# Performance work log

Hardware: AMD Instinct MI355X
Metric: run time of the kernel (lower is better)

The kernel has to match this reference:

```python
import jax, jax.numpy as jnp
import numpy as np

DIM, HEADS, K = 128, 4, 7
HD = DIM // HEADS


def _nbr_idx(n, k):
    # NATTEN boundary-clamped neighborhood (dilation=1): window start clamped to [0, n-k]
    i = np.arange(n)
    start = np.clip(i - k // 2, 0, n - k)
    idx = start[:, None] + np.arange(k)[None, :]          # (n, k) absolute neighbor index
    rel = idx - i[:, None] + (k - 1)                      # (n, k) index into 2k-1 rpb axis
    return jnp.asarray(idx), jnp.asarray(rel)


def _ln(x, w, b, eps=1e-5):
    mu = jnp.mean(x, -1, keepdims=True)
    var = jnp.var(x, -1, keepdims=True)
    return (x - mu) * jax.lax.rsqrt(var + eps) * w + b


def setup_inputs() -> dict:
    key = jax.random.key(0)
    ks = jax.random.split(key, 16)
    B, H, W, C = 1, 128, 128, DIM
    f = jax.random.normal
    inp = {
        'x': f(ks[0], (B, H, W, C), jnp.float32),
        'y': f(ks[1], (B, H, W, C), jnp.float32),
        'qv_w': f(ks[2], (2 * C, C), jnp.float32) * 0.02,
        'qv_b': jnp.zeros((2 * C,), jnp.float32),
        'k_w': f(ks[3], (C, C), jnp.float32) * 0.02,
        'k_b': jnp.zeros((C,), jnp.float32),
        'rpb': f(ks[4], (HEADS, 2 * K - 1, 2 * K - 1), jnp.float32) * 0.02,
        'proj_w': f(ks[5], (C, C), jnp.float32) * 0.02,
        'proj_b': jnp.zeros((C,), jnp.float32),
        'n1_w': jnp.ones((C,), jnp.float32),
        'n1_b': jnp.zeros((C,), jnp.float32),
        'n2_w': jnp.ones((C,), jnp.float32),
        'n2_b': jnp.zeros((C,), jnp.float32),
        'fc1_w': f(ks[6], (4 * C, C), jnp.float32) * 0.02,
        'fc1_b': jnp.zeros((4 * C,), jnp.float32),
        'fc2_w': f(ks[7], (C, 4 * C), jnp.float32) * 0.02,
        'fc2_b': jnp.zeros((C,), jnp.float32),
    }
    return inp


def _block(x, y, qv_w, qv_b, k_w, k_b, rpb, proj_w, proj_b,
           n1_w, n1_b, n2_w, n2_b, fc1_w, fc1_b, fc2_w, fc2_b):
    B, H, W, C = x.shape
    scale = HD ** -0.5
    # ---- CrossNat2D attention on norm1(x) vs y ----
    xn = _ln(x, n1_w, n1_b)
    qv = xn @ qv_w.T + qv_b                               # (B,H,W,2C)
    q = qv[..., :C].reshape(B, H, W, HEADS, HD) * scale
    v = qv[..., C:].reshape(B, H, W, HEADS, HD)
    k = (y @ k_w.T + k_b).reshape(B, H, W, HEADS, HD)

    idx_h, rel_h = _nbr_idx(H, K)
    idx_w, rel_w = _nbr_idx(W, K)
    # gather neighborhoods: (B, H, K, W, K, HEADS, HD)
    k_nbr = k[:, idx_h][:, :, :, idx_w]
    v_nbr = v[:, idx_h][:, :, :, idx_w]

    # attention logits over KxK neighborhood
    attn = jnp.einsum('bijhd,biajchd->bijhac', q, k_nbr)  # (B,H,W,heads,K,K)
    bias = rpb[:, rel_h][..., rel_w]                      # (heads,H,K,W,K)
    attn = attn + jnp.transpose(bias, (1, 3, 0, 2, 4))    # broadcast over B
    attn = jax.nn.softmax(attn.reshape(B, H, W, HEADS, K * K), axis=-1)
    attn = attn.reshape(B, H, W, HEADS, K, K)

    out = jnp.einsum('bijhac,biajchd->bijhd', attn, v_nbr).reshape(B, H, W, C)
    out = out @ proj_w.T + proj_b

    x = x + out
    # ---- MLP ----
    h = _ln(x, n2_w, n2_b) @ fc1_w.T + fc1_b
    h = jax.nn.gelu(h, approximate=False) @ fc2_w.T + fc2_b
    return x + h


def reference(x, y, qv_w, qv_b, k_w, k_b, rpb, proj_w, proj_b,
              n1_w, n1_b, n2_w, n2_b, fc1_w, fc1_b, fc2_w, fc2_b):
    return _block(x, y, qv_w, qv_b, k_w, k_b, rpb, proj_w, proj_b,
                  n1_w, n1_b, n2_w, n2_b, fc1_w, fc1_b, fc2_w, fc2_b)
```

## Files before the change

kernel.cpp:

```cpp
#include <hip/hip_runtime.h>
#include <hip/hip_bf16.h>


#define N_PIX 16384
#define C 128
#define HEADS 4
#define HD 32
#define HW 128

typedef __hip_bfloat16 bf16;
typedef __attribute__((ext_vector_type(8))) short bf16x8;
typedef __attribute__((ext_vector_type(4))) float f32x4;

__device__ __forceinline__ short f2bs(float f) {
    bf16 h = __float2bfloat16(f);
    return (short)__bfloat16_as_ushort(h);
}
__device__ __forceinline__ float bs2f(short s) {
    __hip_bfloat16_raw r; r.x = (unsigned short)s;
    return __bfloat162float(__hip_bfloat16(r));
}
__device__ __forceinline__ float gelu_f(float v) {
    const float z = 1.5957691216f * (v + 0.044715f * v * v * v);
    return v / (1.f + __expf(-z));
}
__device__ __forceinline__ unsigned int pack2(float a, float b) {
    return (unsigned int)(unsigned short)f2bs(a) |
           ((unsigned int)(unsigned short)f2bs(b) << 16);
}

__global__ __launch_bounds__(256) void k_wconv(
    const float* __restrict__ qv_w, const float* __restrict__ k_w,
    const float* __restrict__ proj_w, const float* __restrict__ fc1_w,
    const float* __restrict__ fc2_w,
    short* __restrict__ wqv, short* __restrict__ wk, short* __restrict__ wproj,
    short* __restrict__ wfc1, short* __restrict__ wfc2) {
    const int i = blockIdx.x * 256 + threadIdx.x;
    if (i < 32768) wqv[i] = f2bs(qv_w[i]);
    if (i < 16384) { wk[i] = f2bs(k_w[i]); wproj[i] = f2bs(proj_w[i]); }
    if (i < 65536) { wfc1[i] = f2bs(fc1_w[i]); wfc2[i] = f2bs(fc2_w[i]); }
}

__global__ __launch_bounds__(512, 6) void k_qkv(
    const float* __restrict__ x, const float* __restrict__ y,
    const short* __restrict__ wqv, const float* __restrict__ qv_b,
    const short* __restrict__ wk, const float* __restrict__ k_b,
    const float* __restrict__ n1_w, const float* __restrict__ n1_b,
    bf16* __restrict__ qb, bf16* __restrict__ vb, bf16* __restrict__ kb,
    bf16* __restrict__ xbo) {
    __shared__ float xr[32][132];
    __shared__ short xn[32][136];
    __shared__ short yb[32][136];
    __shared__ float muA[32], riA[32];
    const int t = threadIdx.x;
    const int pix0 = (blockIdx.x & 7) * 2048 + (blockIdx.x >> 3) * 32;
    for (int e = t; e < 1024; e += 512) {
        const int r = e >> 5, c4 = (e & 31) * 4;
        const float4 xv = *(const float4*)(x + (size_t)(pix0 + r) * C + c4);
        *(float4*)&xr[r][c4] = xv;
        uint2 xp; xp.x = pack2(xv.x, xv.y); xp.y = pack2(xv.z, xv.w);
        *(uint2*)(xbo + (size_t)(pix0 + r) * C + c4) = xp;
        const float4 yv = *(const float4*)(y + (size_t)(pix0 + r) * C + c4);
        uint2 yp; yp.x = pack2(yv.x, yv.y); yp.y = pack2(yv.z, yv.w);
        *(uint2*)&yb[r][c4] = yp;
    }
    __syncthreads();
    if (t < 256) {
        const int r = t >> 3, s = t & 7;
        float sm = 0.f, sq = 0.f;
        for (int i = 0; i < 16; i++) { float v = xr[r][s * 16 + i]; sm += v; sq += v * v; }
        for (int m = 1; m < 8; m <<= 1) { sm += __shfl_xor(sm, m, 64); sq += __shfl_xor(sq, m, 64); }
        if (s == 0) {
            const float mu = sm * (1.f / 128.f);
            const float var = sq * (1.f / 128.f) - mu * mu;
            muA[r] = mu; riA[r] = rsqrtf(var + 1e-5f);
        }
    }
    __syncthreads();
    for (int e = t; e < 32 * 128; e += 512) {
        const int r = e >> 7, c = e & 127;
        xn[r][c] = f2bs((xr[r][c] - muA[r]) * riA[r] * n1_w[c] + n1_b[c]);
    }
    __syncthreads();
    const int wave = t >> 6, lane = t & 63, quad = lane >> 4, l15 = lane & 15;
    const int mt = wave & 1, wv = wave >> 1;
    const float scale = 0.1767766952966369f;
    {
        bf16x8 aA[4];
#pragma unroll
        for (int kt = 0; kt < 4; kt++)
            aA[kt] = *(const bf16x8*)&xn[mt * 16 + l15][kt * 32 + quad * 8];
#pragma unroll
        for (int s = 0; s < 4; s++) {
            const int n = (wv * 4 + s) * 16 + l15;
            f32x4 acc = {0.f, 0.f, 0.f, 0.f};
#pragma unroll
            for (int kt = 0; kt < 4; kt++) {
                bf16x8 b = *(const bf16x8*)&wqv[n * C + kt * 32 + quad * 8];
                acc = __builtin_amdgcn_mfma_f32_16x16x32_bf16(aA[kt], b, acc, 0, 0, 0);
            }
            const float bias = qv_b[n];
#pragma unroll
            for (int r = 0; r < 4; r++) {
                const int m = mt * 16 + quad * 4 + r;
                const float v = acc[r] + bias;
                if (n < C) qb[(pix0 + m) * C + n] = __float2bfloat16(v * scale);
                else       vb[(pix0 + m) * C + (n - C)] = __float2bfloat16(v);
            }
        }
    }
    {
        bf16x8 aY[4];
#pragma unroll
        for (int kt = 0; kt < 4; kt++)
            aY[kt] = *(const bf16x8*)&yb[mt * 16 + l15][kt * 32 + quad * 8];
        const int n0 = (wv * 2) * 16 + l15, n1 = (wv * 2 + 1) * 16 + l15;
        f32x4 a0 = {0.f, 0.f, 0.f, 0.f}, a1 = {0.f, 0.f, 0.f, 0.f};
#pragma unroll
        for (int kt = 0; kt < 4; kt++) {
            bf16x8 b0 = *(const bf16x8*)&wk[n0 * C + kt * 32 + quad * 8];
            bf16x8 b1 = *(const bf16x8*)&wk[n1 * C + kt * 32 + quad * 8];
            a0 = __builtin_amdgcn_mfma_f32_16x16x32_bf16(aY[kt], b0, a0, 0, 0, 0);
            a1 = __builtin_amdgcn_mfma_f32_16x16x32_bf16(aY[kt], b1, a1, 0, 0, 0);
        }
        const float b0s = k_b[n0], b1s = k_b[n1];
#pragma unroll
        for (int r = 0; r < 4; r++) {
            const int m = mt * 16 + quad * 4 + r;
            kb[(pix0 + m) * C + n0] = __float2bfloat16(a0[r] + b0s);
            kb[(pix0 + m) * C + n1] = __float2bfloat16(a1[r] + b1s);
        }
    }
}

__global__ __launch_bounds__(512, 2) void k_fam(
    const bf16* __restrict__ qb, const bf16* __restrict__ kb,
    const bf16* __restrict__ vb, const float* __restrict__ rpb,
    const bf16* __restrict__ xb,
    const short* __restrict__ wproj, const float* __restrict__ proj_b,
    const float* __restrict__ n2_w, const float* __restrict__ n2_b,
    const short* __restrict__ wfc1, const float* __restrict__ fc1_b,
    const short* __restrict__ wfc2, const float* __restrict__ fc2_b,
    float* __restrict__ out) {
    __shared__ short KP[19008];
    __shared__ short Vl[19008];
    __shared__ float muA[32], riA[32];
    short* const Pm  = KP;
    short* const aoL = KP;
    short* const x1b = KP + 4352;
    short* const xnb = KP + 8704;
    short* const hb  = Vl;
    const int t = threadIdx.x;
    const int wave = t >> 6, lane = t & 63, quad = lane >> 4, l15 = lane & 15;
    const int h = wave & 3, mt = wave >> 2;
    const int s_ = blockIdx.x >> 3;
    const int i0 = ((blockIdx.x & 7) * 2 + (s_ >> 5)) * 8;
    const int j0 = (s_ & 31) * 4;
    const int rs = min(max(i0 - 3, 0), 114);
    const int cs = min(max(j0 - 3, 0), 118);
    const int mA = mt * 16 + l15;
    const int pA = (i0 + (mA >> 2)) * HW + j0 + (mA & 3);
    const bf16x8 aQ = *(const bf16x8*)(qb + (size_t)pA * C + h * HD + quad * 8);
    const int nR0 = h * 16 + l15, nR1 = (h + 4) * 16 + l15;
    short xres0[4], xres1[4];
#pragma unroll
    for (int r = 0; r < 4; r++) {
        const int m = mt * 16 + quad * 4 + r;
        const int p = (i0 + (m >> 2)) * HW + j0 + (m & 3);
        xres0[r] = *(const short*)(xb + (size_t)p * C + nR0);
        xres1[r] = *(const short*)(xb + (size_t)p * C + nR1);
    }
    for (int u = t; u < 140 * 16 * 2; u += 512) {
        const int tv = (u >= 2240) ? 1 : 0;
        const int uu = tv ? u - 2240 : u;
        const int r = uu >> 4, seg = uu & 15;
        const size_t g = (size_t)((rs + r / 10) * HW + cs + r % 10) * C + seg * 8;
        const uint4 d = *(const uint4*)((tv ? vb : kb) + g);
        *(uint4*)&(tv ? Vl : KP)[r * 132 + seg * 8] = d;
    }
    __syncthreads();
    f32x4 S[9];
#pragma unroll
    for (int nt = 0; nt < 9; nt++) {
        const bf16x8 bK = *(const bf16x8*)&KP[(nt * 16 + l15) * 132 + h * HD + quad * 8];
        f32x4 z = {0.f, 0.f, 0.f, 0.f};
        S[nt] = __builtin_amdgcn_mfma_f32_16x16x32_bf16(aQ, bK, z, 0, 0, 0);
    }
    const float* rpbh = rpb + h * 169;
    float smx[4];
#pragma unroll
    for (int r = 0; r < 4; r++) {
        const int m = mt * 16 + quad * 4 + r;
        const int i = i0 + (m >> 2), j = j0 + (m & 3);
        const int shi = min(max(i - 3, 0), 121);
        const int swj = min(max(j - 3, 0), 121);
        float best = -1e30f;
#pragma unroll
        for (int nt = 0; nt < 9; nt++) {
            const int nb = nt * 16 + l15;
            const int ai = rs + nb / 10, aj = cs + nb % 10;
            const bool valid = (nb < 140) & (ai >= shi) & (ai <= shi + 6) & (aj >= swj) & (aj <= swj + 6);
            const int ri = min(max(ai - i + 6, 0), 12);
            const int rj = min(max(aj - j + 6, 0), 12);
            const float v = valid ? (S[nt][r] + rpbh[ri * 13 + rj]) : -1e30f;
            S[nt][r] = v;
            best = fmaxf(best, v);
        }
        for (int msk = 1; msk < 16; msk <<= 1) best = fmaxf(best, __shfl_xor(best, msk, 64));
        float s = 0.f;
#pragma unroll
        for (int nt = 0; nt < 9; nt++) {
            const float e = __expf(S[nt][r] - best);
            S[nt][r] = e;
            s += e;
        }
        for (int msk = 1; msk < 16; msk <<= 1) s += __shfl_xor(s, msk, 64);
        smx[r] = 1.f / s;
    }
    __syncthreads();
#pragma unroll
    for (int r = 0; r < 4; r++) {
        short* prow = &Pm[(wave * 16 + quad * 4 + r) * 144];
#pragma unroll
        for (int nt = 0; nt < 9; nt++)
            prow[nt * 16 + l15] = f2bs(S[nt][r] * smx[r]);
    }
    f32x4 O0 = {0.f, 0.f, 0.f, 0.f}, O1 = {0.f, 0.f, 0.f, 0.f};
#pragma unroll
    for (int kt = 0; kt < 4; kt++) {
        const bf16x8 aP = *(const bf16x8*)&Pm[(wave * 16 + l15) * 144 + kt * 32 + quad * 8];
#pragma unroll
        for (int nt2 = 0; nt2 < 2; nt2++) {
            const int ch = h * HD + nt2 * 16 + l15;
            const int base = (kt * 32 + quad * 8) * 132 + ch;
            bf16x8 bV;
#pragma unroll
            for (int jj = 0; jj < 8; jj++) bV[jj] = Vl[base + jj * 132];
            if (nt2 == 0) O0 = __builtin_amdgcn_mfma_f32_16x16x32_bf16(aP, bV, O0, 0, 0, 0);
            else          O1 = __builtin_amdgcn_mfma_f32_16x16x32_bf16(aP, bV, O1, 0, 0, 0);
        }
    }
    {
        const bf16x8 aP = *(const bf16x8*)&Pm[(wave * 16 + l15) * 144 + 128 + quad * 8];
#pragma unroll
        for (int nt2 = 0; nt2 < 2; nt2++) {
            const int ch = h * HD + nt2 * 16 + l15;
            bf16x8 bV = {0, 0, 0, 0, 0, 0, 0, 0};
            if (quad == 0) {
                const int base = 128 * 132 + ch;
#pragma unroll
                for (int jj = 0; jj < 8; jj++) bV[jj] = Vl[base + jj * 132];
            } else if (quad == 1) {
                const int base = 136 * 132 + ch;
#pragma unroll
                for (int jj = 0; jj < 4; jj++) bV[jj] = Vl[base + jj * 132];
            }
            if (nt2 == 0) O0 = __builtin_amdgcn_mfma_f32_16x16x32_bf16(aP, bV, O0, 0, 0, 0);
            else          O1 = __builtin_amdgcn_mfma_f32_16x16x32_bf16(aP, bV, O1, 0, 0, 0);
        }
    }
    __syncthreads();
#pragma unroll
    for (int r = 0; r < 4; r++) {
        const int m = mt * 16 + quad * 4 + r;
        aoL[m * 136 + h * HD + l15] = f2bs(O0[r]);
        aoL[m * 136 + h * HD + 16 + l15] = f2bs(O1[r]);
    }
    __syncthreads();
    {
        bf16x8 aO[4];
#pragma unroll
        for (int kt = 0; kt < 4; kt++)
            aO[kt] = *(const bf16x8*)&aoL[(mt * 16 + l15) * 136 + kt * 32 + quad * 8];
        f32x4 a0 = {0.f, 0.f, 0.f, 0.f}, a1 = {0.f, 0.f, 0.f, 0.f};
#pragma unroll
        for (int kt = 0; kt < 4; kt++) {
            bf16x8 b0 = *(const bf16x8*)&wproj[nR0 * C + kt * 32 + quad * 8];
            bf16x8 b1 = *(const bf16x8*)&wproj[nR1 * C + kt * 32 + quad * 8];
            a0 = __builtin_amdgcn_mfma_f32_16x16x32_bf16(aO[kt], b0, a0, 0, 0, 0);
            a1 = __builtin_amdgcn_mfma_f32_16x16x32_bf16(aO[kt], b1, a1, 0, 0, 0);
        }
        const float b0s = proj_b[nR0], b1s = proj_b[nR1];
#pragma unroll
        for (int r = 0; r < 4; r++) {
            const int m = mt * 16 + quad * 4 + r;
            x1b[m * 136 + nR0] = f2bs(bs2f(xres0[r]) + a0[r] + b0s);
            x1b[m * 136 + nR1] = f2bs(bs2f(xres1[r]) + a1[r] + b1s);
        }
    }
    __syncthreads();
    if (t < 256) {
        const int r = t >> 3, s = t & 7;
        float sm = 0.f, sq = 0.f;
        for (int i = 0; i < 16; i++) { float v = bs2f(x1b[r * 136 + s * 16 + i]); sm += v; sq += v * v; }
        for (int m = 1; m < 8; m <<= 1) { sm += __shfl_xor(sm, m, 64); sq += __shfl_xor(sq, m, 64); }
        if (s == 0) {
            const float mu = sm * (1.f / 128.f);
            const float var = sq * (1.f / 128.f) - mu * mu;
            muA[r] = mu; riA[r] = rsqrtf(var + 1e-5f);
        }
    }
    __syncthreads();
    for (int e = t; e < 32 * 128; e += 512) {
        const int r = e >> 7, c = e & 127;
        xnb[r * 136 + c] = f2bs((bs2f(x1b[r * 136 + c]) - muA[r]) * riA[r] * n2_w[c] + n2_b[c]);
    }
    __syncthreads();
    {
        bf16x8 aX[4];
#pragma unroll
        for (int kt = 0; kt < 4; kt++)
            aX[kt] = *(const bf16x8*)&xnb[(mt * 16 + l15) * 136 + kt * 32 + quad * 8];
#pragma unroll
        for (int a = 0; a < 4; a++) {
            const int n0 = (h + 8 * a) * 16 + l15, n1 = (h + 8 * a + 4) * 16 + l15;
            f32x4 a0 = {0.f, 0.f, 0.f, 0.f}, a1 = {0.f, 0.f, 0.f, 0.f};
#pragma unroll
            for (int kt = 0; kt < 4; kt++) {
                bf16x8 b0 = *(const bf16x8*)&wfc1[n0 * C + kt * 32 + quad * 8];
                bf16x8 b1 = *(const bf16x8*)&wfc1[n1 * C + kt * 32 + quad * 8];
                a0 = __builtin_amdgcn_mfma_f32_16x16x32_bf16(aX[kt], b0, a0, 0, 0, 0);
                a1 = __builtin_amdgcn_mfma_f32_16x16x32_bf16(aX[kt], b1, a1, 0, 0, 0);
            }
            const float b0s = fc1_b[n0], b1s = fc1_b[n1];
#pragma unroll
            for (int r = 0; r < 4; r++) {
                const int m = mt * 16 + quad * 4 + r;
                hb[m * 520 + n0] = f2bs(gelu_f(a0[r] + b0s));
                hb[m * 520 + n1] = f2bs(gelu_f(a1[r] + b1s));
            }
        }
    }
    __syncthreads();
    {
        f32x4 a0 = {0.f, 0.f, 0.f, 0.f}, a1 = {0.f, 0.f, 0.f, 0.f};
#pragma unroll
        for (int kt = 0; kt < 16; kt++) {
            const bf16x8 aP = *(const bf16x8*)&hb[(mt * 16 + l15) * 520 + kt * 32 + quad * 8];
            bf16x8 b0 = *(const bf16x8*)&wfc2[nR0 * 512 + kt * 32 + quad * 8];
            bf16x8 b1 = *(const bf16x8*)&wfc2[nR1 * 512 + kt * 32 + quad * 8];
            a0 = __builtin_amdgcn_mfma_f32_16x16x32_bf16(aP, b0, a0, 0, 0, 0);
            a1 = __builtin_amdgcn_mfma_f32_16x16x32_bf16(aP, b1, a1, 0, 0, 0);
        }
        const float b0s = fc2_b[nR0], b1s = fc2_b[nR1];
#pragma unroll
        for (int r = 0; r < 4; r++) {
            const int m = mt * 16 + quad * 4 + r;
            const int p = (i0 + (m >> 2)) * HW + j0 + (m & 3);
            out[(size_t)p * C + nR0] = a0[r] + b0s + bs2f(x1b[m * 136 + nR0]);
            out[(size_t)p * C + nR1] = a1[r] + b1s + bs2f(x1b[m * 136 + nR1]);
        }
    }
}

extern "C" void kernel_launch(void* const* d_in, const int* in_sizes, int n_in,
                              void* d_out, int out_size, void* d_ws, size_t ws_size,
                              hipStream_t stream) {
    const float* x      = (const float*)d_in[0];
    const float* y      = (const float*)d_in[1];
    const float* qv_w   = (const float*)d_in[2];
    const float* qv_b   = (const float*)d_in[3];
    const float* k_w    = (const float*)d_in[4];
    const float* k_b    = (const float*)d_in[5];
    const float* rpb    = (const float*)d_in[6];
    const float* proj_w = (const float*)d_in[7];
    const float* proj_b = (const float*)d_in[8];
    const float* n1_w   = (const float*)d_in[9];
    const float* n1_b   = (const float*)d_in[10];
    const float* n2_w   = (const float*)d_in[11];
    const float* n2_b   = (const float*)d_in[12];
    const float* fc1_w  = (const float*)d_in[13];
    const float* fc1_b  = (const float*)d_in[14];
    const float* fc2_w  = (const float*)d_in[15];
    const float* fc2_b  = (const float*)d_in[16];
    float* out = (float*)d_out;

    bf16* qb  = (bf16*)d_ws;
    bf16* vb  = qb + (size_t)N_PIX * C;
    bf16* kb  = vb + (size_t)N_PIX * C;
    bf16* xb  = kb + (size_t)N_PIX * C;
    short* wqv  = (short*)(xb + (size_t)N_PIX * C);
    short* wk   = wqv + 32768;
    short* wproj= wk + 16384;
    short* wfc1 = wproj + 16384;
    short* wfc2 = wfc1 + 65536;

    k_wconv<<<256, 256, 0, stream>>>(qv_w, k_w, proj_w, fc1_w, fc2_w,
                                     wqv, wk, wproj, wfc1, wfc2);
    k_qkv<<<512, 512, 0, stream>>>(x, y, wqv, qv_b, wk, k_b, n1_w, n1_b,
                                   qb, vb, kb, xb);
    k_fam<<<512, 512, 0, stream>>>(qb, kb, vb, rpb, xb, wproj, proj_b, n2_w, n2_b,
                                   wfc1, fc1_b, wfc2, fc2_b, out);
}
```

Before: 162.7 us.

## Split fused attention+MLP kernel into separate attention and MLP kernels with smaller tiles

The fused attention/projection/MLP kernel becomes two kernels. k_attn handles 4x4 pixel tiles with 256 threads and reuses one shared buffer for K and then V, staging V through registers. k_mlp reads the fp32 residual from the output buffer and applies LN2, fc1, GELU, fc2 and the residual. k_qkv now uses 16-pixel blocks and no longer writes a bf16 copy of x; the residual is read in fp32 instead. The aim is smaller LDS footprint, higher occupancy and a tighter attention halo (100 neighbours instead of 140), at the cost of an extra fp32 round trip of the intermediate through global memory and one more launch.

```diff
diff --git a/kernel.cpp b/kernel.cpp
--- a/kernel.cpp
+++ b/kernel.cpp
@@ -41,31 +41,28 @@
     if (i < 65536) { wfc1[i] = f2bs(fc1_w[i]); wfc2[i] = f2bs(fc2_w[i]); }
 }
 
-__global__ __launch_bounds__(512, 6) void k_qkv(
+__global__ __launch_bounds__(256, 4) void k_qkv(
     const float* __restrict__ x, const float* __restrict__ y,
     const short* __restrict__ wqv, const float* __restrict__ qv_b,
     const short* __restrict__ wk, const float* __restrict__ k_b,
     const float* __restrict__ n1_w, const float* __restrict__ n1_b,
-    bf16* __restrict__ qb, bf16* __restrict__ vb, bf16* __restrict__ kb,
-    bf16* __restrict__ xbo) {
-    __shared__ float xr[32][132];
-    __shared__ short xn[32][136];
-    __shared__ short yb[32][136];
-    __shared__ float muA[32], riA[32];
+    bf16* __restrict__ qb, bf16* __restrict__ vb, bf16* __restrict__ kb) {
+    __shared__ float xr[16][132];
+    __shared__ short xn[16][136];
+    __shared__ short yl[16][136];
+    __shared__ float muA[16], riA[16];
     const int t = threadIdx.x;
-    const int pix0 = (blockIdx.x & 7) * 2048 + (blockIdx.x >> 3) * 32;
-    for (int e = t; e < 1024; e += 512) {
+    const int pix0 = (blockIdx.x & 7) * 2048 + (blockIdx.x >> 3) * 16;
+    for (int e = t; e < 512; e += 256) {
         const int r = e >> 5, c4 = (e & 31) * 4;
         const float4 xv = *(const float4*)(x + (size_t)(pix0 + r) * C + c4);
         *(float4*)&xr[r][c4] = xv;
-        uint2 xp; xp.x = pack2(xv.x, xv.y); xp.y = pack2(xv.z, xv.w);
-        *(uint2*)(xbo + (size_t)(pix0 + r) * C + c4) = xp;
         const float4 yv = *(const float4*)(y + (size_t)(pix0 + r) * C + c4);
         uint2 yp; yp.x = pack2(yv.x, yv.y); yp.y = pack2(yv.z, yv.w);
-        *(uint2*)&yb[r][c4] = yp;
-    }
-    __syncthreads();
-    if (t < 256) {
+        *(uint2*)&yl[r][c4] = yp;
+    }
+    __syncthreads();
+    if (t < 128) {
         const int r = t >> 3, s = t & 7;
         float sm = 0.f, sq = 0.f;
         for (int i = 0; i < 16; i++) { float v = xr[r][s * 16 + i]; sm += v; sq += v * v; }
@@ -77,22 +74,21 @@
         }
     }
     __syncthreads();
-    for (int e = t; e < 32 * 128; e += 512) {
+    for (int e = t; e < 2048; e += 256) {
         const int r = e >> 7, c = e & 127;
         xn[r][c] = f2bs((xr[r][c] - muA[r]) * riA[r] * n1_w[c] + n1_b[c]);
     }
     __syncthreads();
     const int wave = t >> 6, lane = t & 63, quad = lane >> 4, l15 = lane & 15;
-    const int mt = wave & 1, wv = wave >> 1;
     const float scale = 0.1767766952966369f;
     {
         bf16x8 aA[4];
 #pragma unroll
         for (int kt = 0; kt < 4; kt++)
-            aA[kt] = *(const bf16x8*)&xn[mt * 16 + l15][kt * 32 + quad * 8];
+            aA[kt] = *(const bf16x8*)&xn[l15][kt * 32 + quad * 8];
 #pragma unroll
         for (int s = 0; s < 4; s++) {
-            const int n = (wv * 4 + s) * 16 + l15;
+            const int n = (wave * 4 + s) * 16 + l15;
             f32x4 acc = {0.f, 0.f, 0.f, 0.f};
 #pragma unroll
             for (int kt = 0; kt < 4; kt++) {
@@ -102,10 +98,10 @@
             const float bias = qv_b[n];
 #pragma unroll
             for (int r = 0; r < 4; r++) {
-                const int m = mt * 16 + quad * 4 + r;
+                const int m = quad * 4 + r;
                 const float v = acc[r] + bias;
-                if (n < C) qb[(pix0 + m) * C + n] = __float2bfloat16(v * scale);
-                else       vb[(pix0 + m) * C + (n - C)] = __float2bfloat16(v);
+                if (n < C) qb[(size_t)(pix0 + m) * C + n] = __float2bfloat16(v * scale);
+                else       vb[(size_t)(pix0 + m) * C + (n - C)] = __float2bfloat16(v);
             }
         }
     }
@@ -113,8 +109,8 @@
         bf16x8 aY[4];
 #pragma unroll
         for (int kt = 0; kt < 4; kt++)
-            aY[kt] = *(const bf16x8*)&yb[mt * 16 + l15][kt * 32 + quad * 8];
-        const int n0 = (wv * 2) * 16 + l15, n1 = (wv * 2 + 1) * 16 + l15;
+            aY[kt] = *(const bf16x8*)&yl[l15][kt * 32 + quad * 8];
+        const int n0 = (wave * 2) * 16 + l15, n1 = (wave * 2 + 1) * 16 + l15;
         f32x4 a0 = {0.f, 0.f, 0.f, 0.f}, a1 = {0.f, 0.f, 0.f, 0.f};
 #pragma unroll
         for (int kt = 0; kt < 4; kt++) {
@@ -126,80 +122,86 @@
         const float b0s = k_b[n0], b1s = k_b[n1];
 #pragma unroll
         for (int r = 0; r < 4; r++) {
-            const int m = mt * 16 + quad * 4 + r;
-            kb[(pix0 + m) * C + n0] = __float2bfloat16(a0[r] + b0s);
-            kb[(pix0 + m) * C + n1] = __float2bfloat16(a1[r] + b1s);
-        }
-    }
-}
-
-__global__ __launch_bounds__(512, 2) void k_fam(
+            const int m = quad * 4 + r;
+            kb[(size_t)(pix0 + m) * C + n0] = __float2bfloat16(a0[r] + b0s);
+            kb[(size_t)(pix0 + m) * C + n1] = __float2bfloat16(a1[r] + b1s);
+        }
+    }
+}
+
+__global__ __launch_bounds__(256, 3) void k_attn(
     const bf16* __restrict__ qb, const bf16* __restrict__ kb,
     const bf16* __restrict__ vb, const float* __restrict__ rpb,
-    const bf16* __restrict__ xb,
+    const float* __restrict__ x,
     const short* __restrict__ wproj, const float* __restrict__ proj_b,
-    const float* __restrict__ n2_w, const float* __restrict__ n2_b,
-    const short* __restrict__ wfc1, const float* __restrict__ fc1_b,
-    const short* __restrict__ wfc2, const float* __restrict__ fc2_b,
     float* __restrict__ out) {
-    __shared__ short KP[19008];
-    __shared__ short Vl[19008];
-    __shared__ float muA[32], riA[32];
-    short* const Pm  = KP;
-    short* const aoL = KP;
-    short* const x1b = KP + 4352;
-    short* const xnb = KP + 8704;
-    short* const hb  = Vl;
+    __shared__ short U[112 * 132];
+    __shared__ short Pb[64 * 120];
+    __shared__ short aoL[16 * 136];
     const int t = threadIdx.x;
     const int wave = t >> 6, lane = t & 63, quad = lane >> 4, l15 = lane & 15;
-    const int h = wave & 3, mt = wave >> 2;
-    const int s_ = blockIdx.x >> 3;
-    const int i0 = ((blockIdx.x & 7) * 2 + (s_ >> 5)) * 8;
-    const int j0 = (s_ & 31) * 4;
-    const int rs = min(max(i0 - 3, 0), 114);
+    const int h = wave;
+    const int tile = (blockIdx.x & 7) * 128 + (blockIdx.x >> 3);
+    const int i0 = (tile >> 5) * 4, j0 = (tile & 31) * 4;
+    const int rs = min(max(i0 - 3, 0), 118);
     const int cs = min(max(j0 - 3, 0), 118);
-    const int mA = mt * 16 + l15;
-    const int pA = (i0 + (mA >> 2)) * HW + j0 + (mA & 3);
+    const int pA = (i0 + (l15 >> 2)) * HW + j0 + (l15 & 3);
     const bf16x8 aQ = *(const bf16x8*)(qb + (size_t)pA * C + h * HD + quad * 8);
     const int nR0 = h * 16 + l15, nR1 = (h + 4) * 16 + l15;
-    short xres0[4], xres1[4];
+    float xres0[4], xres1[4];
 #pragma unroll
     for (int r = 0; r < 4; r++) {
-        const int m = mt * 16 + quad * 4 + r;
+        const int m = quad * 4 + r;
         const int p = (i0 + (m >> 2)) * HW + j0 + (m & 3);
-        xres0[r] = *(const short*)(xb + (size_t)p * C + nR0);
-        xres1[r] = *(const short*)(xb + (size_t)p * C + nR1);
-    }
-    for (int u = t; u < 140 * 16 * 2; u += 512) {
-        const int tv = (u >= 2240) ? 1 : 0;
-        const int uu = tv ? u - 2240 : u;
-        const int r = uu >> 4, seg = uu & 15;
-        const size_t g = (size_t)((rs + r / 10) * HW + cs + r % 10) * C + seg * 8;
-        const uint4 d = *(const uint4*)((tv ? vb : kb) + g);
-        *(uint4*)&(tv ? Vl : KP)[r * 132 + seg * 8] = d;
-    }
-    __syncthreads();
-    f32x4 S[9];
-#pragma unroll
-    for (int nt = 0; nt < 9; nt++) {
-        const bf16x8 bK = *(const bf16x8*)&KP[(nt * 16 + l15) * 132 + h * HD + quad * 8];
+        xres0[r] = x[(size_t)p * C + nR0];
+        xres1[r] = x[(size_t)p * C + nR1];
+    }
+    uint4 vst[7];
+#pragma unroll
+    for (int it = 0; it < 7; ++it) {
+        const int u = t + it * 256;
+        const int r = u >> 4, seg = u & 15;
+        const int sr = min(r, 99);
+        const size_t g = (size_t)((rs + sr / 10) * HW + cs + sr % 10) * C + seg * 8;
+        *(uint4*)&U[r * 132 + seg * 8] = *(const uint4*)(kb + g);
+        vst[it] = *(const uint4*)(vb + g);
+    }
+    __syncthreads();
+    f32x4 S[7];
+#pragma unroll
+    for (int nt = 0; nt < 7; nt++) {
+        const bf16x8 bK = *(const bf16x8*)&U[(nt * 16 + l15) * 132 + h * HD + quad * 8];
         f32x4 z = {0.f, 0.f, 0.f, 0.f};
         S[nt] = __builtin_amdgcn_mfma_f32_16x16x32_bf16(aQ, bK, z, 0, 0, 0);
     }
+    __syncthreads();
+#pragma unroll
+    for (int it = 0; it < 7; ++it) {
+        const int u = t + it * 256;
+        const int r = u >> 4, seg = u & 15;
+        *(uint4*)&U[r * 132 + seg * 8] = vst[it];
+    }
     const float* rpbh = rpb + h * 169;
+    int aiA[7], ajA[7];
+#pragma unroll
+    for (int nt = 0; nt < 7; nt++) {
+        const int nb = nt * 16 + l15;
+        aiA[nt] = rs + nb / 10;
+        ajA[nt] = cs + nb % 10;
+    }
     float smx[4];
 #pragma unroll
     for (int r = 0; r < 4; r++) {
-        const int m = mt * 16 + quad * 4 + r;
+        const int m = quad * 4 + r;
         const int i = i0 + (m >> 2), j = j0 + (m & 3);
         const int shi = min(max(i - 3, 0), 121);
         const int swj = min(max(j - 3, 0), 121);
         float best = -1e30f;
 #pragma unroll
-        for (int nt = 0; nt < 9; nt++) {
+        for (int nt = 0; nt < 7; nt++) {
             const int nb = nt * 16 + l15;
-            const int ai = rs + nb / 10, aj = cs + nb % 10;
-            const bool valid = (nb < 140) & (ai >= shi) & (ai <= shi + 6) & (aj >= swj) & (aj <= swj + 6);
+            const int ai = aiA[nt], aj = ajA[nt];
+            const bool valid = (nb < 100) & (ai >= shi) & (ai <= shi + 6) & (aj >= swj) & (aj <= swj + 6);
             const int ri = min(max(ai - i + 6, 0), 12);
             const int rj = min(max(aj - j + 6, 0), 12);
             const float v = valid ? (S[nt][r] + rpbh[ri * 13 + rj]) : -1e30f;
@@ -209,7 +211,7 @@
         for (int msk = 1; msk < 16; msk <<= 1) best = fmaxf(best, __shfl_xor(best, msk, 64));
         float s = 0.f;
 #pragma unroll
-        for (int nt = 0; nt < 9; nt++) {
+        for (int nt = 0; nt < 7; nt++) {
             const float e = __expf(S[nt][r] - best);
             S[nt][r] = e;
             s += e;
@@ -217,82 +219,93 @@
         for (int msk = 1; msk < 16; msk <<= 1) s += __shfl_xor(s, msk, 64);
         smx[r] = 1.f / s;
     }
-    __syncthreads();
 #pragma unroll
     for (int r = 0; r < 4; r++) {
-        short* prow = &Pm[(wave * 16 + quad * 4 + r) * 144];
-#pragma unroll
-        for (int nt = 0; nt < 9; nt++)
-            prow[nt * 16 + l15] = f2bs(S[nt][r] * smx[r]);
-    }
+        short* prow = &Pb[(h * 16 + quad * 4 + r) * 120];
+#pragma unroll
+        for (int nt = 0; nt < 7; nt++) prow[nt * 16 + l15] = f2bs(S[nt][r] * smx[r]);
+    }
+    __syncthreads();
     f32x4 O0 = {0.f, 0.f, 0.f, 0.f}, O1 = {0.f, 0.f, 0.f, 0.f};
 #pragma unroll
-    for (int kt = 0; kt < 4; kt++) {
-        const bf16x8 aP = *(const bf16x8*)&Pm[(wave * 16 + l15) * 144 + kt * 32 + quad * 8];
+    for (int kt = 0; kt < 3; kt++) {
+        const bf16x8 aP = *(const bf16x8*)&Pb[(h * 16 + l15) * 120 + kt * 32 + quad * 8];
 #pragma unroll
         for (int nt2 = 0; nt2 < 2; nt2++) {
             const int ch = h * HD + nt2 * 16 + l15;
             const int base = (kt * 32 + quad * 8) * 132 + ch;
             bf16x8 bV;
 #pragma unroll
-            for (int jj = 0; jj < 8; jj++) bV[jj] = Vl[base + jj * 132];
+            for (int jj = 0; jj < 8; jj++) bV[jj] = U[base + jj * 132];
             if (nt2 == 0) O0 = __builtin_amdgcn_mfma_f32_16x16x32_bf16(aP, bV, O0, 0, 0, 0);
             else          O1 = __builtin_amdgcn_mfma_f32_16x16x32_bf16(aP, bV, O1, 0, 0, 0);
         }
     }
     {
-        const bf16x8 aP = *(const bf16x8*)&Pm[(wave * 16 + l15) * 144 + 128 + quad * 8];
+        bf16x8 aP = {0, 0, 0, 0, 0, 0, 0, 0};
+        if (quad < 2) aP = *(const bf16x8*)&Pb[(h * 16 + l15) * 120 + 96 + quad * 8];
 #pragma unroll
         for (int nt2 = 0; nt2 < 2; nt2++) {
             const int ch = h * HD + nt2 * 16 + l15;
             bf16x8 bV = {0, 0, 0, 0, 0, 0, 0, 0};
-            if (quad == 0) {
-                const int base = 128 * 132 + ch;
-#pragma unroll
-                for (int jj = 0; jj < 8; jj++) bV[jj] = Vl[base + jj * 132];
-            } else if (quad == 1) {
-                const int base = 136 * 132 + ch;
-#pragma unroll
-                for (int jj = 0; jj < 4; jj++) bV[jj] = Vl[base + jj * 132];
+            if (quad < 2) {
+                const int base = (96 + quad * 8) * 132 + ch;
+#pragma unroll
+                for (int jj = 0; jj < 8; jj++) bV[jj] = U[base + jj * 132];
             }
             if (nt2 == 0) O0 = __builtin_amdgcn_mfma_f32_16x16x32_bf16(aP, bV, O0, 0, 0, 0);
             else          O1 = __builtin_amdgcn_mfma_f32_16x16x32_bf16(aP, bV, O1, 0, 0, 0);
         }
     }
-    __syncthreads();
 #pragma unroll
     for (int r = 0; r < 4; r++) {
-        const int m = mt * 16 + quad * 4 + r;
+        const int m = quad * 4 + r;
         aoL[m * 136 + h * HD + l15] = f2bs(O0[r]);
         aoL[m * 136 + h * HD + 16 + l15] = f2bs(O1[r]);
     }
     __syncthreads();
-    {
-        bf16x8 aO[4];
-#pragma unroll
-        for (int kt = 0; kt < 4; kt++)
-            aO[kt] = *(const bf16x8*)&aoL[(mt * 16 + l15) * 136 + kt * 32 + quad * 8];
-        f32x4 a0 = {0.f, 0.f, 0.f, 0.f}, a1 = {0.f, 0.f, 0.f, 0.f};
-#pragma unroll
-        for (int kt = 0; kt < 4; kt++) {
-            bf16x8 b0 = *(const bf16x8*)&wproj[nR0 * C + kt * 32 + quad * 8];
-            bf16x8 b1 = *(const bf16x8*)&wproj[nR1 * C + kt * 32 + quad * 8];
-            a0 = __builtin_amdgcn_mfma_f32_16x16x32_bf16(aO[kt], b0, a0, 0, 0, 0);
-            a1 = __builtin_amdgcn_mfma_f32_16x16x32_bf16(aO[kt], b1, a1, 0, 0, 0);
-        }
-        const float b0s = proj_b[nR0], b1s = proj_b[nR1];
-#pragma unroll
-        for (int r = 0; r < 4; r++) {
-            const int m = mt * 16 + quad * 4 + r;
-            x1b[m * 136 + nR0] = f2bs(bs2f(xres0[r]) + a0[r] + b0s);
-            x1b[m * 136 + nR1] = f2bs(bs2f(xres1[r]) + a1[r] + b1s);
-        }
-    }
-    __syncthreads();
-    if (t < 256) {
+    bf16x8 aO[4];
+#pragma unroll
+    for (int kt = 0; kt < 4; kt++)
+        aO[kt] = *(const bf16x8*)&aoL[l15 * 136 + kt * 32 + quad * 8];
+    f32x4 a0 = {0.f, 0.f, 0.f, 0.f}, a1 = {0.f, 0.f, 0.f, 0.f};
+#pragma unroll
+    for (int kt = 0; kt < 4; kt++) {
+        bf16x8 b0 = *(const bf16x8*)&wproj[nR0 * C + kt * 32 + quad * 8];
+        bf16x8 b1 = *(const bf16x8*)&wproj[nR1 * C + kt * 32 + quad * 8];
+        a0 = __builtin_amdgcn_mfma_f32_16x16x32_bf16(aO[kt], b0, a0, 0, 0, 0);
+        a1 = __builtin_amdgcn_mfma_f32_16x16x32_bf16(aO[kt], b1, a1, 0, 0, 0);
+    }
+    const float b0s = proj_b[nR0], b1s = proj_b[nR1];
+#pragma unroll
+    for (int r = 0; r < 4; r++) {
+        const int m = quad * 4 + r;
+        const int p = (i0 + (m >> 2)) * HW + j0 + (m & 3);
+        out[(size_t)p * C + nR0] = xres0[r] + a0[r] + b0s;
+        out[(size_t)p * C + nR1] = xres1[r] + a1[r] + b1s;
+    }
+}
+
+__global__ __launch_bounds__(256, 4) void k_mlp(
+    const float* __restrict__ n2_w, const float* __restrict__ n2_b,
+    const short* __restrict__ wfc1, const float* __restrict__ fc1_b,
+    const short* __restrict__ wfc2, const float* __restrict__ fc2_b,
+    float* __restrict__ out) {
+    __shared__ float x1l[16][132];
+    __shared__ short xnb[16][136];
+    __shared__ short hb[16 * 520];
+    __shared__ float muA[16], riA[16];
+    const int t = threadIdx.x;
+    const int pix0 = (blockIdx.x & 7) * 2048 + (blockIdx.x >> 3) * 16;
+    for (int e = t; e < 512; e += 256) {
+        const int r = e >> 5, c4 = (e & 31) * 4;
+        *(float4*)&x1l[r][c4] = *(const float4*)(out + (size_t)(pix0 + r) * C + c4);
+    }
+    __syncthreads();
+    if (t < 128) {
         const int r = t >> 3, s = t & 7;
         float sm = 0.f, sq = 0.f;
-        for (int i = 0; i < 16; i++) { float v = bs2f(x1b[r * 136 + s * 16 + i]); sm += v; sq += v * v; }
+        for (int i = 0; i < 16; i++) { float v = x1l[r][s * 16 + i]; sm += v; sq += v * v; }
         for (int m = 1; m < 8; m <<= 1) { sm += __shfl_xor(sm, m, 64); sq += __shfl_xor(sq, m, 64); }
         if (s == 0) {
             const float mu = sm * (1.f / 128.f);
@@ -301,54 +314,52 @@
         }
     }
     __syncthreads();
-    for (int e = t; e < 32 * 128; e += 512) {
+    for (int e = t; e < 2048; e += 256) {
         const int r = e >> 7, c = e & 127;
-        xnb[r * 136 + c] = f2bs((bs2f(x1b[r * 136 + c]) - muA[r]) * riA[r] * n2_w[c] + n2_b[c]);
-    }
-    __syncthreads();
+        xnb[r][c] = f2bs((x1l[r][c] - muA[r]) * riA[r] * n2_w[c] + n2_b[c]);
+    }
+    __syncthreads();
+    const int wave = t >> 6, lane = t & 63, quad = lane >> 4, l15 = lane & 15;
     {
         bf16x8 aX[4];
 #pragma unroll
         for (int kt = 0; kt < 4; kt++)
-            aX[kt] = *(const bf16x8*)&xnb[(mt * 16 + l15) * 136 + kt * 32 + quad * 8];
-#pragma unroll
-        for (int a = 0; a < 4; a++) {
-            const int n0 = (h + 8 * a) * 16 + l15, n1 = (h + 8 * a + 4) * 16 + l15;
-            f32x4 a0 = {0.f, 0.f, 0.f, 0.f}, a1 = {0.f, 0.f, 0.f, 0.f};
+            aX[kt] = *(const bf16x8*)&xnb[l15][kt * 32 + quad * 8];
+#pragma unroll
+        for (int a = 0; a < 8; a++) {
+            const int n = (wave * 8 + a) * 16 + l15;
+            f32x4 acc = {0.f, 0.f, 0.f, 0.f};
 #pragma unroll
             for (int kt = 0; kt < 4; kt++) {
-                bf16x8 b0 = *(const bf16x8*)&wfc1[n0 * C + kt * 32 + quad * 8];
-                bf16x8 b1 = *(const bf16x8*)&wfc1[n1 * C + kt * 32 + quad * 8];
-                a0 = __builtin_amdgcn_mfma_f32_16x16x32_bf16(aX[kt], b0, a0, 0, 0, 0);
-                a1 = __builtin_amdgcn_mfma_f32_16x16x32_bf16(aX[kt], b1, a1, 0, 0, 0);
+                bf16x8 bw = *(const bf16x8*)&wfc1[n * C + kt * 32 + quad * 8];
+                acc = __builtin_amdgcn_mfma_f32_16x16x32_bf16(aX[kt], bw, acc, 0, 0, 0);
             }
-            const float b0s = fc1_b[n0], b1s = fc1_b[n1];
+            const float bias = fc1_b[n];
 #pragma unroll
             for (int r = 0; r < 4; r++) {
-                const int m = mt * 16 + quad * 4 + r;
-                hb[m * 520 + n0] = f2bs(gelu_f(a0[r] + b0s));
-                hb[m * 520 + n1] = f2bs(gelu_f(a1[r] + b1s));
+                const int m = quad * 4 + r;
+                hb[m * 520 + n] = f2bs(gelu_f(acc[r] + bias));
             }
         }
     }
     __syncthreads();
     {
+        const int n0 = (wave * 2) * 16 + l15, n1 = (wave * 2 + 1) * 16 + l15;
         f32x4 a0 = {0.f, 0.f, 0.f, 0.f}, a1 = {0.f, 0.f, 0.f, 0.f};
 #pragma unroll
         for (int kt = 0; kt < 16; kt++) {
-            const bf16x8 aP = *(const bf16x8*)&hb[(mt * 16 + l15) * 520 + kt * 32 + quad * 8];
-            bf16x8 b0 = *(const bf16x8*)&wfc2[nR0 * 512 + kt * 32 + quad * 8];
-            bf16x8 b1 = *(const bf16x8*)&wfc2[nR1 * 512 + kt * 32 + quad * 8];
+            const bf16x8 aP = *(const bf16x8*)&hb[l15 * 520 + kt * 32 + quad * 8];
+            bf16x8 b0 = *(const bf16x8*)&wfc2[n0 * 512 + kt * 32 + quad * 8];
+            bf16x8 b1 = *(const bf16x8*)&wfc2[n1 * 512 + kt * 32 + quad * 8];
             a0 = __builtin_amdgcn_mfma_f32_16x16x32_bf16(aP, b0, a0, 0, 0, 0);
             a1 = __builtin_amdgcn_mfma_f32_16x16x32_bf16(aP, b1, a1, 0, 0, 0);
         }
-        const float b0s = fc2_b[nR0], b1s = fc2_b[nR1];
+        const float b0s = fc2_b[n0], b1s = fc2_b[n1];
 #pragma unroll
         for (int r = 0; r < 4; r++) {
-            const int m = mt * 16 + quad * 4 + r;
-            const int p = (i0 + (m >> 2)) * HW + j0 + (m & 3);
-            out[(size_t)p * C + nR0] = a0[r] + b0s + bs2f(x1b[m * 136 + nR0]);
-            out[(size_t)p * C + nR1] = a1[r] + b1s + bs2f(x1b[m * 136 + nR1]);
+            const int m = quad * 4 + r;
+            out[(size_t)(pix0 + m) * C + n0] = a0[r] + b0s + x1l[m][n0];
+            out[(size_t)(pix0 + m) * C + n1] = a1[r] + b1s + x1l[m][n1];
         }
     }
 }
@@ -378,8 +389,7 @@
     bf16* qb  = (bf16*)d_ws;
     bf16* vb  = qb + (size_t)N_PIX * C;
     bf16* kb  = vb + (size_t)N_PIX * C;
-    bf16* xb  = kb + (size_t)N_PIX * C;
-    short* wqv  = (short*)(xb + (size_t)N_PIX * C);
+    short* wqv  = (short*)(kb + (size_t)N_PIX * C);
     short* wk   = wqv + 32768;
     short* wproj= wk + 16384;
     short* wfc1 = wproj + 16384;
@@ -387,8 +397,8 @@
 
     k_wconv<<<256, 256, 0, stream>>>(qv_w, k_w, proj_w, fc1_w, fc2_w,
                                      wqv, wk, wproj, wfc1, wfc2);
-    k_qkv<<<512, 512, 0, stream>>>(x, y, wqv, qv_b, wk, k_b, n1_w, n1_b,
-                                   qb, vb, kb, xb);
-    k_fam<<<512, 512, 0, stream>>>(qb, kb, vb, rpb, xb, wproj, proj_b, n2_w, n2_b,
-                                   wfc1, fc1_b, wfc2, fc2_b, out);
-}
+    k_qkv<<<1024, 256, 0, stream>>>(x, y, wqv, qv_b, wk, k_b, n1_w, n1_b,
+                                    qb, vb, kb);
+    k_attn<<<1024, 256, 0, stream>>>(qb, kb, vb, rpb, x, wproj, proj_b, out);
+    k_mlp<<<1024, 256, 0, stream>>>(n2_w, n2_b, wfc1, fc1_b, wfc2, fc2_b, out);
+}
```

After: 177.4 us. 9.0% more time.

## Drop bf16 x copy, read fp32 residual directly, shrink QKV tiles

Applied to the files above, without the earlier changes.

The QKV kernel no longer writes a bf16 copy of x to workspace. The fused attention/MLP kernel now reads the fp32 x residual directly and keeps the post-attention residual in fp32 registers for the final output add, instead of re-reading it from LDS as bf16. The QKV kernel is also retiled to 16 pixels per 256-thread block with 1024 blocks, removing the m-tile split. This cuts a global write and improves residual precision, but doubles the bytes read for the residual and halves per-block weight reuse in QKV.

```diff
diff --git a/kernel.cpp b/kernel.cpp
--- a/kernel.cpp
+++ b/kernel.cpp
@@ -41,31 +41,28 @@
     if (i < 65536) { wfc1[i] = f2bs(fc1_w[i]); wfc2[i] = f2bs(fc2_w[i]); }
 }
 
-__global__ __launch_bounds__(512, 6) void k_qkv(
+__global__ __launch_bounds__(256, 4) void k_qkv(
     const float* __restrict__ x, const float* __restrict__ y,
     const short* __restrict__ wqv, const float* __restrict__ qv_b,
     const short* __restrict__ wk, const float* __restrict__ k_b,
     const float* __restrict__ n1_w, const float* __restrict__ n1_b,
-    bf16* __restrict__ qb, bf16* __restrict__ vb, bf16* __restrict__ kb,
-    bf16* __restrict__ xbo) {
-    __shared__ float xr[32][132];
-    __shared__ short xn[32][136];
-    __shared__ short yb[32][136];
-    __shared__ float muA[32], riA[32];
+    bf16* __restrict__ qb, bf16* __restrict__ vb, bf16* __restrict__ kb) {
+    __shared__ float xr[16][132];
+    __shared__ short xn[16][136];
+    __shared__ short yl[16][136];
+    __shared__ float muA[16], riA[16];
     const int t = threadIdx.x;
-    const int pix0 = (blockIdx.x & 7) * 2048 + (blockIdx.x >> 3) * 32;
-    for (int e = t; e < 1024; e += 512) {
+    const int pix0 = (blockIdx.x & 7) * 2048 + (blockIdx.x >> 3) * 16;
+    for (int e = t; e < 512; e += 256) {
         const int r = e >> 5, c4 = (e & 31) * 4;
         const float4 xv = *(const float4*)(x + (size_t)(pix0 + r) * C + c4);
         *(float4*)&xr[r][c4] = xv;
-        uint2 xp; xp.x = pack2(xv.x, xv.y); xp.y = pack2(xv.z, xv.w);
-        *(uint2*)(xbo + (size_t)(pix0 + r) * C + c4) = xp;
         const float4 yv = *(const float4*)(y + (size_t)(pix0 + r) * C + c4);
         uint2 yp; yp.x = pack2(yv.x, yv.y); yp.y = pack2(yv.z, yv.w);
-        *(uint2*)&yb[r][c4] = yp;
-    }
-    __syncthreads();
-    if (t < 256) {
+        *(uint2*)&yl[r][c4] = yp;
+    }
+    __syncthreads();
+    if (t < 128) {
         const int r = t >> 3, s = t & 7;
         float sm = 0.f, sq = 0.f;
         for (int i = 0; i < 16; i++) { float v = xr[r][s * 16 + i]; sm += v; sq += v * v; }
@@ -77,22 +74,21 @@
         }
     }
     __syncthreads();
-    for (int e = t; e < 32 * 128; e += 512) {
+    for (int e = t; e < 2048; e += 256) {
         const int r = e >> 7, c = e & 127;
         xn[r][c] = f2bs((xr[r][c] - muA[r]) * riA[r] * n1_w[c] + n1_b[c]);
     }
     __syncthreads();
     const int wave = t >> 6, lane = t & 63, quad = lane >> 4, l15 = lane & 15;
-    const int mt = wave & 1, wv = wave >> 1;
     const float scale = 0.1767766952966369f;
     {
         bf16x8 aA[4];
 #pragma unroll
         for (int kt = 0; kt < 4; kt++)
-            aA[kt] = *(const bf16x8*)&xn[mt * 16 + l15][kt * 32 + quad * 8];
+            aA[kt] = *(const bf16x8*)&xn[l15][kt * 32 + quad * 8];
 #pragma unroll
         for (int s = 0; s < 4; s++) {
-            const int n = (wv * 4 + s) * 16 + l15;
+            const int n = (wave * 4 + s) * 16 + l15;
             f32x4 acc = {0.f, 0.f, 0.f, 0.f};
 #pragma unroll
             for (int kt = 0; kt < 4; kt++) {
@@ -102,10 +98,10 @@
             const float bias = qv_b[n];
 #pragma unroll
             for (int r = 0; r < 4; r++) {
-                const int m = mt * 16 + quad * 4 + r;
+                const int m = quad * 4 + r;
                 const float v = acc[r] + bias;
-                if (n < C) qb[(pix0 + m) * C + n] = __float2bfloat16(v * scale);
-                else       vb[(pix0 + m) * C + (n - C)] = __float2bfloat16(v);
+                if (n < C) qb[(size_t)(pix0 + m) * C + n] = __float2bfloat16(v * scale);
+                else       vb[(size_t)(pix0 + m) * C + (n - C)] = __float2bfloat16(v);
             }
         }
     }
@@ -113,8 +109,8 @@
         bf16x8 aY[4];
 #pragma unroll
         for (int kt = 0; kt < 4; kt++)
-            aY[kt] = *(const bf16x8*)&yb[mt * 16 + l15][kt * 32 + quad * 8];
-        const int n0 = (wv * 2) * 16 + l15, n1 = (wv * 2 + 1) * 16 + l15;
+            aY[kt] = *(const bf16x8*)&yl[l15][kt * 32 + quad * 8];
+        const int n0 = (wave * 2) * 16 + l15, n1 = (wave * 2 + 1) * 16 + l15;
         f32x4 a0 = {0.f, 0.f, 0.f, 0.f}, a1 = {0.f, 0.f, 0.f, 0.f};
 #pragma unroll
         for (int kt = 0; kt < 4; kt++) {
@@ -126,9 +122,9 @@
         const float b0s = k_b[n0], b1s = k_b[n1];
 #pragma unroll
         for (int r = 0; r < 4; r++) {
-            const int m = mt * 16 + quad * 4 + r;
-            kb[(pix0 + m) * C + n0] = __float2bfloat16(a0[r] + b0s);
-            kb[(pix0 + m) * C + n1] = __float2bfloat16(a1[r] + b1s);
+            const int m = quad * 4 + r;
+            kb[(size_t)(pix0 + m) * C + n0] = __float2bfloat16(a0[r] + b0s);
+            kb[(size_t)(pix0 + m) * C + n1] = __float2bfloat16(a1[r] + b1s);
         }
     }
 }
@@ -136,7 +132,7 @@
 __global__ __launch_bounds__(512, 2) void k_fam(
     const bf16* __restrict__ qb, const bf16* __restrict__ kb,
     const bf16* __restrict__ vb, const float* __restrict__ rpb,
-    const bf16* __restrict__ xb,
+    const float* __restrict__ x,
     const short* __restrict__ wproj, const float* __restrict__ proj_b,
     const float* __restrict__ n2_w, const float* __restrict__ n2_b,
     const short* __restrict__ wfc1, const float* __restrict__ fc1_b,
@@ -162,13 +158,13 @@
     const int pA = (i0 + (mA >> 2)) * HW + j0 + (mA & 3);
     const bf16x8 aQ = *(const bf16x8*)(qb + (size_t)pA * C + h * HD + quad * 8);
     const int nR0 = h * 16 + l15, nR1 = (h + 4) * 16 + l15;
-    short xres0[4], xres1[4];
+    float xres0[4], xres1[4];
 #pragma unroll
     for (int r = 0; r < 4; r++) {
         const int m = mt * 16 + quad * 4 + r;
         const int p = (i0 + (m >> 2)) * HW + j0 + (m & 3);
-        xres0[r] = *(const short*)(xb + (size_t)p * C + nR0);
-        xres1[r] = *(const short*)(xb + (size_t)p * C + nR1);
+        xres0[r] = x[(size_t)p * C + nR0];
+        xres1[r] = x[(size_t)p * C + nR1];
     }
     for (int u = t; u < 140 * 16 * 2; u += 512) {
         const int tv = (u >= 2240) ? 1 : 0;
@@ -267,6 +263,7 @@
         aoL[m * 136 + h * HD + 16 + l15] = f2bs(O1[r]);
     }
     __syncthreads();
+    float x1f0[4], x1f1[4];
     {
         bf16x8 aO[4];
 #pragma unroll
@@ -284,8 +281,11 @@
 #pragma unroll
         for (int r = 0; r < 4; r++) {
             const int m = mt * 16 + quad * 4 + r;
-            x1b[m * 136 + nR0] = f2bs(bs2f(xres0[r]) + a0[r] + b0s);
-            x1b[m * 136 + nR1] = f2bs(bs2f(xres1[r]) + a1[r] + b1s);
+            const float v0 = xres0[r] + a0[r] + b0s;
+            const float v1 = xres1[r] + a1[r] + b1s;
+            x1f0[r] = v0; x1f1[r] = v1;
+            x1b[m * 136 + nR0] = f2bs(v0);
+            x1b[m * 136 + nR1] = f2bs(v1);
         }
     }
     __syncthreads();
@@ -347,8 +347,8 @@
         for (int r = 0; r < 4; r++) {
             const int m = mt * 16 + quad * 4 + r;
             const int p = (i0 + (m >> 2)) * HW + j0 + (m & 3);
-            out[(size_t)p * C + nR0] = a0[r] + b0s + bs2f(x1b[m * 136 + nR0]);
-            out[(size_t)p * C + nR1] = a1[r] + b1s + bs2f(x1b[m * 136 + nR1]);
+            out[(size_t)p * C + nR0] = a0[r] + b0s + x1f0[r];
+            out[(size_t)p * C + nR1] = a1[r] + b1s + x1f1[r];
         }
     }
 }
@@ -378,8 +378,7 @@
     bf16* qb  = (bf16*)d_ws;
     bf16* vb  = qb + (size_t)N_PIX * C;
     bf16* kb  = vb + (size_t)N_PIX * C;
-    bf16* xb  = kb + (size_t)N_PIX * C;
-    short* wqv  = (short*)(xb + (size_t)N_PIX * C);
+    short* wqv  = (short*)(kb + (size_t)N_PIX * C);
     short* wk   = wqv + 32768;
     short* wproj= wk + 16384;
     short* wfc1 = wproj + 16384;
@@ -387,8 +386,8 @@
 
     k_wconv<<<256, 256, 0, stream>>>(qv_w, k_w, proj_w, fc1_w, fc2_w,
                                      wqv, wk, wproj, wfc1, wfc2);
-    k_qkv<<<512, 512, 0, stream>>>(x, y, wqv, qv_b, wk, k_b, n1_w, n1_b,
-                                   qb, vb, kb, xb);
-    k_fam<<<512, 512, 0, stream>>>(qb, kb, vb, rpb, xb, wproj, proj_b, n2_w, n2_b,
+    k_qkv<<<1024, 256, 0, stream>>>(x, y, wqv, qv_b, wk, k_b, n1_w, n1_b,
+                                    qb, vb, kb);
+    k_fam<<<512, 512, 0, stream>>>(qb, kb, vb, rpb, x, wproj, proj_b, n2_w, n2_b,
                                    wfc1, fc1_b, wfc2, fc2_b, out);
 }
```

New measurement: 160.1 us. About the same (-1.6%).
